# Optimization experiments

Hardware: AMD Instinct MI355X
Metric: run time of the kernel (lower is better)

The kernel has to match this reference:

```python
import jax, jax.numpy as jnp
import numpy as np

N_NODES = 100000
N_EDGES = 1600000
D_IN = 128
D_OUT = 128


def setup_inputs() -> dict:
    key = jax.random.key(0)
    kx, ke, kw = jax.random.split(key, 3)
    x = jax.random.normal(kx, (N_NODES, D_IN), dtype=jnp.float32)
    edge_index = jax.random.randint(ke, (2, N_EDGES), 0, N_NODES, dtype=jnp.int32)
    W = jax.random.normal(kw, (D_IN, D_OUT), dtype=jnp.float32) / np.sqrt(D_IN)
    b = jnp.zeros((D_OUT,), dtype=jnp.float32)
    return {"x": x, "edge_index": edge_index, "W": W, "b": b}


def reference(x, edge_index, W, b):
    # PyG GCNConv: x' = D^{-1/2} (A + I) D^{-1/2} (x @ W) + b, then ReLU.
    n = x.shape[0]
    xw = x @ W  # linear transform first (as in GCNConv)
    # add self-loops
    loops = jnp.arange(n, dtype=edge_index.dtype)
    row = jnp.concatenate([edge_index[0], loops])  # source nodes
    col = jnp.concatenate([edge_index[1], loops])  # destination nodes
    # symmetric degree normalization (degree counted on destination, PyG-style)
    deg = jax.ops.segment_sum(jnp.ones_like(col, dtype=xw.dtype), col, num_segments=n)
    dinv = jnp.where(deg > 0, jax.lax.rsqrt(deg), 0.0)
    norm = dinv[row] * dinv[col]  # [E+N]
    # gather -> scale -> scatter-add
    msg = xw[row] * norm[:, None]  # [E+N, D_OUT]
    agg = jax.ops.segment_sum(msg, col, num_segments=n)  # [N, D_OUT]
    return jax.nn.relu(agg + b)
```

## Files before the change

### kernel.cpp

```cpp
#include <hip/hip_runtime.h>

#define DCH 128
#define T_PART 4096
#define B_MAX 512
#define CAPC 6144

typedef short bf16x8 __attribute__((ext_vector_type(8)));
typedef float f32x4 __attribute__((ext_vector_type(4)));

__device__ inline unsigned short f2bf(float f) {
    unsigned int u = __float_as_uint(f);
    unsigned int r = (u + 0x7fffu + ((u >> 16) & 1u)) >> 16;
    return (unsigned short)r;
}

__global__ __launch_bounds__(256) void k_init(const float* __restrict__ W,
                                              unsigned short* __restrict__ Wf,
                                              int* __restrict__ gcount, int B) {
    int idx = blockIdx.x * 256 + threadIdx.x;
    if (idx < B) gcount[idx] = 0;
    int frag = blockIdx.x * 4 + (threadIdx.x >> 6);
    if (frag < 32) {
        int lane = threadIdx.x & 63;
        int nt = frag >> 2, ks = frag & 3;
        int nn = nt * 16 + (lane & 15);
        int k0 = ks * 32 + ((lane >> 4) * 8);
        unsigned short tmp[8];
#pragma unroll
        for (int j = 0; j < 8; ++j) tmp[j] = f2bf(W[(size_t)(k0 + j) * DCH + nn]);
        *(uint4*)&Wf[((size_t)frag * 64 + lane) * 8] = *(const uint4*)tmp;
    }
}

__global__ __launch_bounds__(512) void k_part(const int* __restrict__ row,
                                              const int* __restrict__ col,
                                              unsigned int* __restrict__ coarse,
                                              int* __restrict__ gcount,
                                              int E, int B) {
    __shared__ int hist[B_MAX];
    __shared__ int basex[B_MAX];
    __shared__ int curx[B_MAX];
    __shared__ int gb[B_MAX];
    __shared__ int wsum[8];
    __shared__ unsigned int spack[T_PART];
    __shared__ unsigned short sbuck[T_PART];

    int tid = threadIdx.x;
    int wv = tid >> 6, lane = tid & 63;
    int base_e = blockIdx.x * T_PART;
    int tileCnt = min(T_PART, E - base_e);

    hist[tid] = 0;
    __syncthreads();

    int er[8], ec[8];
#pragma unroll
    for (int i = 0; i < 8; ++i) {
        int e = base_e + tid + i * 512;
        if (e < E) {
            er[i] = row[e];
            ec[i] = col[e];
            atomicAdd(&hist[ec[i] >> 8], 1);
        } else {
            er[i] = -1;
            ec[i] = 0;
        }
    }
    __syncthreads();

    int v = hist[tid];
    int x = v;
#pragma unroll
    for (int o = 1; o < 64; o <<= 1) {
        int t = __shfl_up(x, o, 64);
        if (lane >= o) x += t;
    }
    if (lane == 63) wsum[wv] = x;
    __syncthreads();
    int add = 0;
    for (int w = 0; w < wv; ++w) add += wsum[w];
    int excl = x - v + add;
    basex[tid] = excl;
    curx[tid] = excl;
    if (tid < B) gb[tid] = (v > 0) ? atomicAdd(&gcount[tid], v) : 0;
    else gb[tid] = 0;
    __syncthreads();

#pragma unroll
    for (int i = 0; i < 8; ++i) {
        if (er[i] >= 0) {
            int b = ec[i] >> 8;
            int slot = atomicAdd(&curx[b], 1);
            spack[slot] = ((unsigned int)er[i] << 8) | (unsigned int)(ec[i] & 255);
            sbuck[slot] = (unsigned short)b;
        }
    }
    __syncthreads();

    for (int s = tid; s < tileCnt; s += 512) {
        int b = sbuck[s];
        int dst = gb[b] + (s - basex[b]);
        if (dst < CAPC) coarse[(size_t)b * CAPC + dst] = spack[s];
    }
}

__global__ __launch_bounds__(512) void k_csr(const unsigned int* __restrict__ coarse,
                                             const int* __restrict__ gcount,
                                             int* __restrict__ srow,
                                             int* __restrict__ off,
                                             int* __restrict__ cnt,
                                             int n, int B) {
    __shared__ unsigned int ent[CAPC];
    __shared__ int h[256], cur[256];
    __shared__ int red1[8], red2[4];
    __shared__ int bbase_s;

    int b = blockIdx.x;
    int tid = threadIdx.x;
    int wv = tid >> 6, lane = tid & 63;

    int part = 0;
    for (int i = tid; i < b; i += 512) part += gcount[i];
#pragma unroll
    for (int o = 1; o < 64; o <<= 1) part += __shfl_xor(part, o, 64);
    if (lane == 0) red1[wv] = part;
    if (tid < 256) h[tid] = 0;
    __syncthreads();
    if (tid == 0) {
        int s = 0;
        for (int w = 0; w < 8; ++w) s += red1[w];
        bbase_s = s;
    }
    int cntb = min(gcount[b], CAPC);
    for (int s = tid; s < cntb; s += 512) ent[s] = coarse[(size_t)b * CAPC + s];
    __syncthreads();

    for (int s = tid; s < cntb; s += 512) atomicAdd(&h[ent[s] & 255], 1);
    __syncthreads();

    int x = 0, v = 0;
    if (tid < 256) {
        v = h[tid];
        x = v;
#pragma unroll
        for (int o = 1; o < 64; o <<= 1) {
            int t = __shfl_up(x, o, 64);
            if (lane >= o) x += t;
        }
        if (lane == 63) red2[wv] = x;
    }
    __syncthreads();
    if (tid < 256) {
        int add = 0;
        for (int w = 0; w < wv; ++w) add += red2[w];
        int excl = x - v + add;
        cur[tid] = excl;
        int node = (b << 8) + tid;
        if (node < n) {
            cnt[node] = v;
            off[node] = bbase_s + excl;
        }
    }
    __syncthreads();

    int bbase = bbase_s;
    for (int s = tid; s < cntb; s += 512) {
        unsigned int p = ent[s];
        int d = p & 255;
        int slot = atomicAdd(&cur[d], 1);
        srow[bbase + slot] = (int)(p >> 8);
    }
}

__global__ __launch_bounds__(256) void k_gemm_mfma(const float* __restrict__ x,
                                                   const unsigned short* __restrict__ Wf,
                                                   const int* __restrict__ cnt,
                                                   unsigned short* __restrict__ y,
                                                   int n) {
    int tid = threadIdx.x;
    int wv = tid >> 6;
    int lane = tid & 63;
    int rowBase = blockIdx.x * 64 + wv * 16;
    int m = rowBase + (lane & 15);
    int mc = (m < n) ? m : (n - 1);
    int kq = (lane >> 4) * 8;

    f32x4 acc[8];
    f32x4 zero = {0.f, 0.f, 0.f, 0.f};
#pragma unroll
    for (int t = 0; t < 8; ++t) acc[t] = zero;

    const bf16x8* wfv = (const bf16x8*)Wf;
#pragma unroll
    for (int ks = 0; ks < 4; ++ks) {
        int kbase = ks * 32 + kq;
        float4 lo = *(const float4*)&x[(size_t)mc * DCH + kbase];
        float4 hi = *(const float4*)&x[(size_t)mc * DCH + kbase + 4];
        bf16x8 a;
        a[0] = (short)f2bf(lo.x); a[1] = (short)f2bf(lo.y);
        a[2] = (short)f2bf(lo.z); a[3] = (short)f2bf(lo.w);
        a[4] = (short)f2bf(hi.x); a[5] = (short)f2bf(hi.y);
        a[6] = (short)f2bf(hi.z); a[7] = (short)f2bf(hi.w);
#pragma unroll
        for (int nt = 0; nt < 8; ++nt) {
            bf16x8 bfr = wfv[(nt * 4 + ks) * 64 + lane];
            acc[nt] = __builtin_amdgcn_mfma_f32_16x16x32_bf16(a, bfr, acc[nt], 0, 0, 0);
        }
    }

    int orow_base = rowBase + ((lane >> 4) * 4);
#pragma unroll
    for (int r = 0; r < 4; ++r) {
        int orow = orow_base + r;
        if (orow < n) {
            float s = rsqrtf((float)(cnt[orow] + 1));
#pragma unroll
            for (int nt = 0; nt < 8; ++nt) {
                y[(size_t)orow * DCH + nt * 16 + (lane & 15)] = f2bf(acc[nt][r] * s);
            }
        }
    }
}

__global__ __launch_bounds__(256) void k_agg(const uint4* __restrict__ y4,
                                             const int* __restrict__ srow,
                                             const int* __restrict__ off,
                                             const float* __restrict__ b,
                                             float* __restrict__ out, int n, int E) {
    int i = blockIdx.x * 4 + (threadIdx.x >> 6);
    if (i >= n) return;
    int lane = threadIdx.x & 63;
    int q = lane >> 4;
    int l16 = lane & 15;
    int s = off[i];
    int e = (i + 1 < n) ? off[i + 1] : E;

    float acc[8];
#pragma unroll
    for (int k = 0; k < 8; ++k) acc[k] = 0.f;

    if (q == 0) {
        uint4 v = y4[(size_t)i * 16 + l16];
        unsigned int p[4] = {v.x, v.y, v.z, v.w};
#pragma unroll
        for (int t = 0; t < 4; ++t) {
            acc[2 * t]     += __uint_as_float(p[t] << 16);
            acc[2 * t + 1] += __uint_as_float(p[t] & 0xffff0000u);
        }
    }

    int j = s;
    for (; j + 8 <= e; j += 8) {
        int s0 = srow[j + q];
        int s1 = srow[j + 4 + q];
        uint4 v0 = y4[(size_t)s0 * 16 + l16];
        uint4 v1 = y4[(size_t)s1 * 16 + l16];
        unsigned int p0[4] = {v0.x, v0.y, v0.z, v0.w};
        unsigned int p1[4] = {v1.x, v1.y, v1.z, v1.w};
#pragma unroll
        for (int t = 0; t < 4; ++t) {
            acc[2 * t]     += __uint_as_float(p0[t] << 16);
            acc[2 * t + 1] += __uint_as_float(p0[t] & 0xffff0000u);
            acc[2 * t]     += __uint_as_float(p1[t] << 16);
            acc[2 * t + 1] += __uint_as_float(p1[t] & 0xffff0000u);
        }
    }
    for (; j + 4 <= e; j += 4) {
        int s0 = srow[j + q];
        uint4 v0 = y4[(size_t)s0 * 16 + l16];
        unsigned int p0[4] = {v0.x, v0.y, v0.z, v0.w};
#pragma unroll
        for (int t = 0; t < 4; ++t) {
            acc[2 * t]     += __uint_as_float(p0[t] << 16);
            acc[2 * t + 1] += __uint_as_float(p0[t] & 0xffff0000u);
        }
    }
    if (j + q < e) {
        int s0 = srow[j + q];
        uint4 v0 = y4[(size_t)s0 * 16 + l16];
        unsigned int p0[4] = {v0.x, v0.y, v0.z, v0.w};
#pragma unroll
        for (int t = 0; t < 4; ++t) {
            acc[2 * t]     += __uint_as_float(p0[t] << 16);
            acc[2 * t + 1] += __uint_as_float(p0[t] & 0xffff0000u);
        }
    }

#pragma unroll
    for (int k = 0; k < 8; ++k) {
        acc[k] += __shfl_xor(acc[k], 16, 64);
        acc[k] += __shfl_xor(acc[k], 32, 64);
    }

    if (q == 0) {
        float sc = rsqrtf((float)(e - s + 1));
        int c0 = l16 * 8;
        float4 b0 = *(const float4*)&b[c0];
        float4 b1 = *(const float4*)&b[c0 + 4];
        float4 o0, o1;
        o0.x = fmaxf(fmaf(sc, acc[0], b0.x), 0.f);
        o0.y = fmaxf(fmaf(sc, acc[1], b0.y), 0.f);
        o0.z = fmaxf(fmaf(sc, acc[2], b0.z), 0.f);
        o0.w = fmaxf(fmaf(sc, acc[3], b0.w), 0.f);
        o1.x = fmaxf(fmaf(sc, acc[4], b1.x), 0.f);
        o1.y = fmaxf(fmaf(sc, acc[5], b1.y), 0.f);
        o1.z = fmaxf(fmaf(sc, acc[6], b1.z), 0.f);
        o1.w = fmaxf(fmaf(sc, acc[7], b1.w), 0.f);
        float4* orow = (float4*)&out[(size_t)i * DCH + c0];
        orow[0] = o0;
        orow[1] = o1;
    }
}

extern "C" void kernel_launch(void* const* d_in, const int* in_sizes, int n_in,
                              void* d_out, int out_size, void* d_ws, size_t ws_size,
                              hipStream_t stream) {
    const float* x = (const float*)d_in[0];
    const int* ei  = (const int*)d_in[1];
    const float* W = (const float*)d_in[2];
    const float* b = (const float*)d_in[3];
    float* out = (float*)d_out;

    int n = in_sizes[0] / DCH;
    int E = in_sizes[1] / 2;
    const int* row = ei;
    const int* col = ei + E;

    int B = (n + 255) / 256;

    char* ws = (char*)d_ws;
    size_t o = 0;
    auto alloc = [&](size_t bytes) -> void* {
        o = (o + 255) & ~(size_t)255;
        void* p = ws + o;
        o += bytes;
        return p;
    };
    int* cnt     = (int*)alloc((size_t)n * 4);
    int* off     = (int*)alloc((size_t)(n + 1) * 4);
    int* gcount  = (int*)alloc((size_t)B * 4);
    int* srow    = (int*)alloc((size_t)E * 4);
    unsigned int* coarse = (unsigned int*)alloc((size_t)B * CAPC * 4);
    unsigned short* Wf = (unsigned short*)alloc((size_t)DCH * DCH * 2);
    unsigned short* y  = (unsigned short*)alloc((size_t)n * DCH * 2);

    int nt = (E + T_PART - 1) / T_PART;
    k_init<<<8, 256, 0, stream>>>(W, Wf, gcount, B);
    k_part<<<nt, 512, 0, stream>>>(row, col, coarse, gcount, E, B);
    k_csr<<<B, 512, 0, stream>>>(coarse, gcount, srow, off, cnt, n, B);
    k_gemm_mfma<<<(n + 63) / 64, 256, 0, stream>>>(x, Wf, cnt, y, n);
    k_agg<<<(n + 3) / 4, 256, 0, stream>>>((const uint4*)y, srow, off, b, out, n, E);
}
```

Measured before the change: 213.7 us.

## Fuse init, partition, CSR build and GEMM into one cooperative kernel

Merges the four preprocessing and GEMM kernels into a single persistent cooperative kernel that uses grid-wide syncs between phases, removing separate kernel launches and their gaps. Destination buckets grow to 512 nodes, the partition tile and block size shrink to 2048 edges and 256 threads, and the per-bucket offset scan now reads the coarse buffer directly from global memory instead of staging it in LDS. Grid barriers and a fixed persistent grid can serialize phases and leave CUs idle on small phases. Larger buckets also raise the capacity and overflow risk (CAPC 10240).

```diff
diff --git a/kernel.cpp b/kernel.cpp
--- a/kernel.cpp
+++ b/kernel.cpp
@@ -1,9 +1,12 @@
 #include <hip/hip_runtime.h>
+#include <hip/hip_cooperative_groups.h>
+
+namespace cg = cooperative_groups;
 
 #define DCH 128
-#define T_PART 4096
-#define B_MAX 512
-#define CAPC 6144
+#define TPB 256
+#define T_PART 2048
+#define CAPC 10240
 
 typedef short bf16x8 __attribute__((ext_vector_type(8)));
 typedef float f32x4 __attribute__((ext_vector_type(4)));
@@ -14,14 +17,36 @@
     return (unsigned short)r;
 }
 
-__global__ __launch_bounds__(256) void k_init(const float* __restrict__ W,
-                                              unsigned short* __restrict__ Wf,
-                                              int* __restrict__ gcount, int B) {
-    int idx = blockIdx.x * 256 + threadIdx.x;
-    if (idx < B) gcount[idx] = 0;
-    int frag = blockIdx.x * 4 + (threadIdx.x >> 6);
-    if (frag < 32) {
-        int lane = threadIdx.x & 63;
+union SMem {
+    struct {
+        int hist[256], basex[256], curx[256], gb[256], wsum[4];
+        unsigned int spack[T_PART];
+        unsigned char sbuck[T_PART];
+    } p1;
+    struct {
+        int base_[513];
+        int cur_[512];
+        int red[4];
+        int bbase;
+    } p2;
+};
+
+__global__ __launch_bounds__(TPB, 4) void k_mega(
+        const float* __restrict__ x, const int* __restrict__ row,
+        const int* __restrict__ col, const float* __restrict__ W,
+        unsigned short* __restrict__ Wf, int* __restrict__ cnt,
+        int* __restrict__ off, int* __restrict__ gcount,
+        unsigned int* __restrict__ coarse, int* __restrict__ srow,
+        unsigned short* __restrict__ y, int n, int E, int B, int ntiles, int nrt) {
+    __shared__ SMem sm;
+    cg::grid_group grid = cg::this_grid();
+
+    int tid = threadIdx.x;
+    int wv = tid >> 6, lane = tid & 63;
+
+    if (blockIdx.x == 0 && tid < B) gcount[tid] = 0;
+    if (blockIdx.x >= 1 && blockIdx.x <= 8) {
+        int frag = (blockIdx.x - 1) * 4 + wv;
         int nt = frag >> 2, ks = frag & 3;
         int nn = nt * 16 + (lane & 15);
         int k0 = ks * 32 + ((lane >> 4) * 8);
@@ -30,193 +55,175 @@
         for (int j = 0; j < 8; ++j) tmp[j] = f2bf(W[(size_t)(k0 + j) * DCH + nn]);
         *(uint4*)&Wf[((size_t)frag * 64 + lane) * 8] = *(const uint4*)tmp;
     }
-}
-
-__global__ __launch_bounds__(512) void k_part(const int* __restrict__ row,
-                                              const int* __restrict__ col,
-                                              unsigned int* __restrict__ coarse,
-                                              int* __restrict__ gcount,
-                                              int E, int B) {
-    __shared__ int hist[B_MAX];
-    __shared__ int basex[B_MAX];
-    __shared__ int curx[B_MAX];
-    __shared__ int gb[B_MAX];
-    __shared__ int wsum[8];
-    __shared__ unsigned int spack[T_PART];
-    __shared__ unsigned short sbuck[T_PART];
-
-    int tid = threadIdx.x;
-    int wv = tid >> 6, lane = tid & 63;
-    int base_e = blockIdx.x * T_PART;
-    int tileCnt = min(T_PART, E - base_e);
-
-    hist[tid] = 0;
-    __syncthreads();
-
-    int er[8], ec[8];
-#pragma unroll
-    for (int i = 0; i < 8; ++i) {
-        int e = base_e + tid + i * 512;
-        if (e < E) {
-            er[i] = row[e];
-            ec[i] = col[e];
-            atomicAdd(&hist[ec[i] >> 8], 1);
-        } else {
-            er[i] = -1;
-            ec[i] = 0;
-        }
-    }
-    __syncthreads();
-
-    int v = hist[tid];
-    int x = v;
-#pragma unroll
-    for (int o = 1; o < 64; o <<= 1) {
-        int t = __shfl_up(x, o, 64);
-        if (lane >= o) x += t;
-    }
-    if (lane == 63) wsum[wv] = x;
-    __syncthreads();
-    int add = 0;
-    for (int w = 0; w < wv; ++w) add += wsum[w];
-    int excl = x - v + add;
-    basex[tid] = excl;
-    curx[tid] = excl;
-    if (tid < B) gb[tid] = (v > 0) ? atomicAdd(&gcount[tid], v) : 0;
-    else gb[tid] = 0;
-    __syncthreads();
-
-#pragma unroll
-    for (int i = 0; i < 8; ++i) {
-        if (er[i] >= 0) {
-            int b = ec[i] >> 8;
-            int slot = atomicAdd(&curx[b], 1);
-            spack[slot] = ((unsigned int)er[i] << 8) | (unsigned int)(ec[i] & 255);
-            sbuck[slot] = (unsigned short)b;
-        }
-    }
-    __syncthreads();
-
-    for (int s = tid; s < tileCnt; s += 512) {
-        int b = sbuck[s];
-        int dst = gb[b] + (s - basex[b]);
-        if (dst < CAPC) coarse[(size_t)b * CAPC + dst] = spack[s];
-    }
-}
-
-__global__ __launch_bounds__(512) void k_csr(const unsigned int* __restrict__ coarse,
-                                             const int* __restrict__ gcount,
-                                             int* __restrict__ srow,
-                                             int* __restrict__ off,
-                                             int* __restrict__ cnt,
-                                             int n, int B) {
-    __shared__ unsigned int ent[CAPC];
-    __shared__ int h[256], cur[256];
-    __shared__ int red1[8], red2[4];
-    __shared__ int bbase_s;
-
-    int b = blockIdx.x;
-    int tid = threadIdx.x;
-    int wv = tid >> 6, lane = tid & 63;
-
-    int part = 0;
-    for (int i = tid; i < b; i += 512) part += gcount[i];
-#pragma unroll
-    for (int o = 1; o < 64; o <<= 1) part += __shfl_xor(part, o, 64);
-    if (lane == 0) red1[wv] = part;
-    if (tid < 256) h[tid] = 0;
-    __syncthreads();
-    if (tid == 0) {
-        int s = 0;
-        for (int w = 0; w < 8; ++w) s += red1[w];
-        bbase_s = s;
-    }
-    int cntb = min(gcount[b], CAPC);
-    for (int s = tid; s < cntb; s += 512) ent[s] = coarse[(size_t)b * CAPC + s];
-    __syncthreads();
-
-    for (int s = tid; s < cntb; s += 512) atomicAdd(&h[ent[s] & 255], 1);
-    __syncthreads();
-
-    int x = 0, v = 0;
-    if (tid < 256) {
-        v = h[tid];
-        x = v;
+    __threadfence();
+    grid.sync();
+
+    for (int tile = blockIdx.x; tile < ntiles; tile += gridDim.x) {
+        int base_e = tile * T_PART;
+        int tileCnt = min(T_PART, E - base_e);
+
+        sm.p1.hist[tid] = 0;
+        __syncthreads();
+
+        int er[8], ec[8];
+#pragma unroll
+        for (int i = 0; i < 8; ++i) {
+            int e = base_e + tid + i * TPB;
+            if (e < E) {
+                er[i] = row[e];
+                ec[i] = col[e];
+                atomicAdd(&sm.p1.hist[ec[i] >> 9], 1);
+            } else {
+                er[i] = -1;
+                ec[i] = 0;
+            }
+        }
+        __syncthreads();
+
+        int v = sm.p1.hist[tid];
+        int xs = v;
 #pragma unroll
         for (int o = 1; o < 64; o <<= 1) {
-            int t = __shfl_up(x, o, 64);
-            if (lane >= o) x += t;
-        }
-        if (lane == 63) red2[wv] = x;
-    }
-    __syncthreads();
-    if (tid < 256) {
+            int t = __shfl_up(xs, o, 64);
+            if (lane >= o) xs += t;
+        }
+        if (lane == 63) sm.p1.wsum[wv] = xs;
+        __syncthreads();
         int add = 0;
-        for (int w = 0; w < wv; ++w) add += red2[w];
-        int excl = x - v + add;
-        cur[tid] = excl;
-        int node = (b << 8) + tid;
-        if (node < n) {
-            cnt[node] = v;
-            off[node] = bbase_s + excl;
-        }
-    }
-    __syncthreads();
-
-    int bbase = bbase_s;
-    for (int s = tid; s < cntb; s += 512) {
-        unsigned int p = ent[s];
-        int d = p & 255;
-        int slot = atomicAdd(&cur[d], 1);
-        srow[bbase + slot] = (int)(p >> 8);
-    }
-}
-
-__global__ __launch_bounds__(256) void k_gemm_mfma(const float* __restrict__ x,
-                                                   const unsigned short* __restrict__ Wf,
-                                                   const int* __restrict__ cnt,
-                                                   unsigned short* __restrict__ y,
-                                                   int n) {
-    int tid = threadIdx.x;
-    int wv = tid >> 6;
-    int lane = tid & 63;
-    int rowBase = blockIdx.x * 64 + wv * 16;
-    int m = rowBase + (lane & 15);
-    int mc = (m < n) ? m : (n - 1);
-    int kq = (lane >> 4) * 8;
-
-    f32x4 acc[8];
-    f32x4 zero = {0.f, 0.f, 0.f, 0.f};
-#pragma unroll
-    for (int t = 0; t < 8; ++t) acc[t] = zero;
+        for (int w = 0; w < wv; ++w) add += sm.p1.wsum[w];
+        int excl = xs - v + add;
+        sm.p1.basex[tid] = excl;
+        sm.p1.curx[tid] = excl;
+        sm.p1.gb[tid] = (tid < B && v > 0) ? atomicAdd(&gcount[tid], v) : 0;
+        __syncthreads();
+
+#pragma unroll
+        for (int i = 0; i < 8; ++i) {
+            if (er[i] >= 0) {
+                int bk = ec[i] >> 9;
+                int slot = atomicAdd(&sm.p1.curx[bk], 1);
+                sm.p1.spack[slot] = ((unsigned int)er[i] << 9) | (unsigned int)(ec[i] & 511);
+                sm.p1.sbuck[slot] = (unsigned char)bk;
+            }
+        }
+        __syncthreads();
+
+        for (int s = tid; s < tileCnt; s += TPB) {
+            int bk = sm.p1.sbuck[s];
+            int dst = sm.p1.gb[bk] + (s - sm.p1.basex[bk]);
+            if (dst < CAPC) coarse[(size_t)bk * CAPC + dst] = sm.p1.spack[s];
+        }
+        __syncthreads();
+    }
+    __threadfence();
+    grid.sync();
+
+    for (int bk = blockIdx.x; bk < B; bk += gridDim.x) {
+        int part = 0;
+        for (int i = tid; i < bk; i += TPB) part += min(gcount[i], CAPC);
+#pragma unroll
+        for (int o = 1; o < 64; o <<= 1) part += __shfl_xor(part, o, 64);
+        if (lane == 0) sm.p2.red[wv] = part;
+        sm.p2.cur_[tid] = 0;
+        sm.p2.cur_[tid + 256] = 0;
+        __syncthreads();
+        if (tid == 0)
+            sm.p2.bbase = sm.p2.red[0] + sm.p2.red[1] + sm.p2.red[2] + sm.p2.red[3];
+        int cntb = min(gcount[bk], CAPC);
+        __syncthreads();
+
+        const unsigned int* cbase = &coarse[(size_t)bk * CAPC];
+        for (int s = tid; s < cntb; s += TPB)
+            atomicAdd(&sm.p2.cur_[cbase[s] & 511], 1);
+        __syncthreads();
+
+        if (tid < 64) {
+            int loc[8];
+            int run = 0;
+#pragma unroll
+            for (int k = 0; k < 8; ++k) { run += sm.p2.cur_[8 * tid + k]; loc[k] = run; }
+            int tot = run, sc = run;
+#pragma unroll
+            for (int o = 1; o < 64; o <<= 1) {
+                int t = __shfl_up(sc, o, 64);
+                if (tid >= o) sc += t;
+            }
+            int lex = sc - tot;
+#pragma unroll
+            for (int k = 0; k < 8; ++k)
+                sm.p2.base_[8 * tid + k] = lex + loc[k] - sm.p2.cur_[8 * tid + k];
+            if (tid == 63) sm.p2.base_[512] = lex + tot;
+        }
+        __syncthreads();
+
+        int bbase = sm.p2.bbase;
+#pragma unroll
+        for (int h = 0; h < 2; ++h) {
+            int d = tid + 256 * h;
+            int node = (bk << 9) + d;
+            if (node < n) {
+                cnt[node] = sm.p2.cur_[d];
+                off[node] = bbase + sm.p2.base_[d];
+            }
+        }
+        __syncthreads();
+#pragma unroll
+        for (int h = 0; h < 2; ++h) {
+            int d = tid + 256 * h;
+            sm.p2.cur_[d] = sm.p2.base_[d];
+        }
+        __syncthreads();
+
+        for (int s = tid; s < cntb; s += TPB) {
+            unsigned int p = cbase[s];
+            int d = p & 511;
+            int slot = atomicAdd(&sm.p2.cur_[d], 1);
+            srow[bbase + slot] = (int)(p >> 9);
+        }
+        __syncthreads();
+    }
+    __threadfence();
+    grid.sync();
 
     const bf16x8* wfv = (const bf16x8*)Wf;
-#pragma unroll
-    for (int ks = 0; ks < 4; ++ks) {
-        int kbase = ks * 32 + kq;
-        float4 lo = *(const float4*)&x[(size_t)mc * DCH + kbase];
-        float4 hi = *(const float4*)&x[(size_t)mc * DCH + kbase + 4];
-        bf16x8 a;
-        a[0] = (short)f2bf(lo.x); a[1] = (short)f2bf(lo.y);
-        a[2] = (short)f2bf(lo.z); a[3] = (short)f2bf(lo.w);
-        a[4] = (short)f2bf(hi.x); a[5] = (short)f2bf(hi.y);
-        a[6] = (short)f2bf(hi.z); a[7] = (short)f2bf(hi.w);
-#pragma unroll
-        for (int nt = 0; nt < 8; ++nt) {
-            bf16x8 bfr = wfv[(nt * 4 + ks) * 64 + lane];
-            acc[nt] = __builtin_amdgcn_mfma_f32_16x16x32_bf16(a, bfr, acc[nt], 0, 0, 0);
-        }
-    }
-
-    int orow_base = rowBase + ((lane >> 4) * 4);
-#pragma unroll
-    for (int r = 0; r < 4; ++r) {
-        int orow = orow_base + r;
-        if (orow < n) {
-            float s = rsqrtf((float)(cnt[orow] + 1));
+    for (int rt = blockIdx.x; rt < nrt; rt += gridDim.x) {
+        int rowBase = rt * 64 + wv * 16;
+        int m = rowBase + (lane & 15);
+        int mc = (m < n) ? m : (n - 1);
+        int kq = (lane >> 4) * 8;
+
+        f32x4 acc[8];
+        f32x4 zero = {0.f, 0.f, 0.f, 0.f};
+#pragma unroll
+        for (int t = 0; t < 8; ++t) acc[t] = zero;
+
+#pragma unroll
+        for (int ks = 0; ks < 4; ++ks) {
+            int kbase = ks * 32 + kq;
+            float4 lo = *(const float4*)&x[(size_t)mc * DCH + kbase];
+            float4 hi = *(const float4*)&x[(size_t)mc * DCH + kbase + 4];
+            bf16x8 a;
+            a[0] = (short)f2bf(lo.x); a[1] = (short)f2bf(lo.y);
+            a[2] = (short)f2bf(lo.z); a[3] = (short)f2bf(lo.w);
+            a[4] = (short)f2bf(hi.x); a[5] = (short)f2bf(hi.y);
+            a[6] = (short)f2bf(hi.z); a[7] = (short)f2bf(hi.w);
 #pragma unroll
             for (int nt = 0; nt < 8; ++nt) {
-                y[(size_t)orow * DCH + nt * 16 + (lane & 15)] = f2bf(acc[nt][r] * s);
+                bf16x8 bfr = wfv[(nt * 4 + ks) * 64 + lane];
+                acc[nt] = __builtin_amdgcn_mfma_f32_16x16x32_bf16(a, bfr, acc[nt], 0, 0, 0);
+            }
+        }
+
+        int orow_base = rowBase + ((lane >> 4) * 4);
+#pragma unroll
+        for (int r = 0; r < 4; ++r) {
+            int orow = orow_base + r;
+            if (orow < n) {
+                float s = rsqrtf((float)(cnt[orow] + 1));
+#pragma unroll
+                for (int nt = 0; nt < 8; ++nt) {
+                    y[(size_t)orow * DCH + nt * 16 + (lane & 15)] = f2bf(acc[nt][r] * s);
+                }
             }
         }
     }
@@ -326,7 +333,9 @@
     const int* row = ei;
     const int* col = ei + E;
 
-    int B = (n + 255) / 256;
+    int B = (n + 511) >> 9;
+    int ntiles = (E + T_PART - 1) / T_PART;
+    int nrt = (n + 63) / 64;
 
     char* ws = (char*)d_ws;
     size_t o = 0;
@@ -344,10 +353,17 @@
     unsigned short* Wf = (unsigned short*)alloc((size_t)DCH * DCH * 2);
     unsigned short* y  = (unsigned short*)alloc((size_t)n * DCH * 2);
 
-    int nt = (E + T_PART - 1) / T_PART;
-    k_init<<<8, 256, 0, stream>>>(W, Wf, gcount, B);
-    k_part<<<nt, 512, 0, stream>>>(row, col, coarse, gcount, E, B);
-    k_csr<<<B, 512, 0, stream>>>(coarse, gcount, srow, off, cnt, n, B);
-    k_gemm_mfma<<<(n + 63) / 64, 256, 0, stream>>>(x, Wf, cnt, y, n);
+    int occ = 4;
+    hipOccupancyMaxActiveBlocksPerMultiprocessor(&occ, (const void*)k_mega, TPB, 0);
+    int grid = occ * 256;
+    if (grid > 1024) grid = 1024;
+    if (grid < 256) grid = 256;
+
+    void* args[] = { (void*)&x, (void*)&row, (void*)&col, (void*)&W, (void*)&Wf,
+                     (void*)&cnt, (void*)&off, (void*)&gcount, (void*)&coarse,
+                     (void*)&srow, (void*)&y, (void*)&n, (void*)&E, (void*)&B,
+                     (void*)&ntiles, (void*)&nrt };
+    hipLaunchCooperativeKernel((const void*)k_mega, dim3(grid), dim3(TPB),
+                               args, 0, stream);
     k_agg<<<(n + 3) / 4, 256, 0, stream>>>((const uint4*)y, srow, off, b, out, n, E);
 }
```

Result: slower. 551.6 us (+158.1%).
